# Performance work log

Hardware: AMD Instinct MI355X
Metric: run time of the kernel (lower is better)

## Reference

```python
import jax, jax.numpy as jnp
import numpy as np

IT = 3  # BP iterations
ROWS, N = 144, 576  # H dims: wman_N0576_R34 -> 144 checks, 576 vars
ROW_DEG = 6  # check-node degree


def _make_H():
    rng = np.random.default_rng(0)
    H = np.zeros((ROWS, N), np.float32)
    for i in range(ROWS):
        cols = rng.choice(N, size=ROW_DEG, replace=False)
        H[i, cols] = 1.0
    return jnp.asarray(H)


def _quantize(x, eta, qk):
    # 4-level soft quantization: softmax over -(x-qk)^2/(2 eta^2)
    logits = -(x[..., None] - qk) ** 2 / (2.0 * eta ** 2 + 1e-12)
    w = jax.nn.softmax(logits, axis=-1)
    return jnp.sum(w * qk, axis=-1)


def setup_inputs() -> dict:
    key = jax.random.key(0)
    k1, = jax.random.split(key, 1)
    batch = 512
    r = jax.random.normal(k1, (batch, N), dtype=jnp.float32)
    H = _make_H()
    alpha = jnp.ones((IT,), jnp.float32) * 0.7
    beta = jnp.ones((IT,), jnp.float32) * 0.05
    eta = jnp.ones((IT,), jnp.float32) * 0.7
    qk = jnp.linspace(-4.0, 4.0, 4).astype(jnp.float32)
    return {"r": r, "H": H, "alpha": alpha, "beta": beta, "eta": eta, "qk": qk}


def reference(r, H, alpha, beta, eta, qk):
    B, n = r.shape
    Hmask = H == 1
    node_idx = jnp.arange(n)[None, None, :]
    M = H[None] * r[:, None, :]          # (B, ROWS, N)
    E = jnp.zeros_like(M)
    for t in range(IT):
        # --- check-to-variable (min-sum with masked top-2) ---
        masked_abs = jnp.where(Hmask, jnp.abs(M), jnp.inf)
        neg_top, idx = jax.lax.top_k(-masked_abs, 2)  # two smallest
        min1 = -neg_top[..., 0:1]
        min2 = -neg_top[..., 1:2]
        idx1 = idx[..., 0:1]
        E_abs = jnp.where(node_idx == idx1, min2, min1)
        signs = jnp.sign(M)
        valid_signs = jnp.where(Hmask, signs, 1.0)
        row_sign_prod = jnp.prod(valid_signs, axis=2, keepdims=True)
        E_sign = row_sign_prod * valid_signs
        E = alpha[t] * E_sign * jnp.maximum(0.0, E_abs - beta[t])
        E = E * H
        E = _quantize(E, eta[t], qk)
        # --- variable-to-check update ---
        sum_E = jnp.sum(E, axis=1, keepdims=True)
        M = (r[:, None, :] + sum_E - E) * H[None]
        M = _quantize(M, eta[t], qk)
    return r + jnp.sum(E, axis=1)
```

## Files before the change

kernel.cpp:

```cpp
#include <hip/hip_runtime.h>
#include <math.h>

#define IT 3
#define ROWS 144
#define NCOLS 576
#define ROW_DEG 6

__device__ __forceinline__ float quantize1(float x, float S,
                                           float K0, float K1, float K2, float K3,
                                           float KQ0, float KQ1, float KQ2, float KQ3) {
    float s = fminf(fmaxf(x * S, -30.0f), 30.0f);
    float B = __expf(s);
    float den = ((K3 * B + K2) * B + K1) * B + K0;
    float num = ((KQ3 * B + KQ2) * B + KQ1) * B + KQ0;
    return num * __builtin_amdgcn_rcpf(den);
}

__device__ __forceinline__ float signf(float x) {
    return (x > 0.0f) ? 1.0f : ((x < 0.0f) ? -1.0f : 0.0f);
}

__global__ __launch_bounds__(64) void extract_cols_kernel(
    const float* __restrict__ H, int* __restrict__ cols)
{
    const int row  = blockIdx.x;
    const int lane = threadIdx.x;
    float hv[9];
    #pragma unroll
    for (int i = 0; i < 9; ++i) hv[i] = H[row * NCOLS + i * 64 + lane];
    int base = 0;
    #pragma unroll
    for (int i = 0; i < 9; ++i) {
        bool nz = hv[i] != 0.0f;
        unsigned long long mask = __ballot(nz);
        if (nz) {
            int rank = base + __popcll(mask & ((1ull << lane) - 1ull));
            if (rank < ROW_DEG) cols[row * ROW_DEG + rank] = i * 64 + lane;
        }
        base += __popcll(mask);
    }
}

__global__ __launch_bounds__(64) void decode_kernel(
    const float* __restrict__ r, const int* __restrict__ cols,
    const float* __restrict__ alpha, const float* __restrict__ beta,
    const float* __restrict__ eta, const float* __restrict__ qk,
    float* __restrict__ out)
{
    __shared__ __align__(16) float s_r[NCOLS];
    __shared__ __align__(16) float s_sumE[NCOLS];

    const int b    = blockIdx.x;
    const int lane = threadIdx.x;

    const float q0 = qk[0], q1 = qk[1], q2 = qk[2], q3 = qk[3];

    const float4* rb4 = reinterpret_cast<const float4*>(r + (size_t)b * NCOLS);
    float4* s_r4 = reinterpret_cast<float4*>(s_r);
    #pragma unroll
    for (int p = 0; p < 3; ++p) {
        int j = lane + 64 * p;
        if (j < NCOLS / 4) s_r4[j] = rb4[j];
    }

    const float dq = (q3 - q0) * (1.0f / 3.0f);
    float al[IT], be[IT], sc[IT];
    float k0[IT], k1[IT], k2[IT], k3[IT];
    #pragma unroll
    for (int t = 0; t < IT; ++t) {
        al[t] = alpha[t];
        be[t] = beta[t];
        float inv2e = 1.0f / (2.0f * eta[t] * eta[t] + 1e-12f);
        sc[t] = 2.0f * dq * inv2e;
        k0[t] = __expf(-q0 * q0 * inv2e);
        k1[t] = __expf(-q1 * q1 * inv2e);
        k2[t] = __expf(-q2 * q2 * inv2e);
        k3[t] = __expf(-q3 * q3 * inv2e);
    }

    const bool act2 = lane < (ROWS - 128);

    int   c[3][ROW_DEG];
    float m[3][ROW_DEG];
    float E[3][ROW_DEG];

    __syncthreads();

    #pragma unroll
    for (int p = 0; p < 3; ++p) {
        if (p == 2 && !act2) continue;
        const int row = lane + 64 * p;
        #pragma unroll
        for (int e = 0; e < ROW_DEG; ++e) {
            c[p][e] = cols[row * ROW_DEG + e];
            m[p][e] = s_r[c[p][e]];
        }
    }

    #pragma unroll
    for (int t = 0; t < IT; ++t) {
        __syncthreads();
        #pragma unroll
        for (int p = 0; p < 9; ++p) s_sumE[lane + 64 * p] = 0.0f;
        __syncthreads();

        const float A = al[t], Bt = be[t], S = sc[t];
        const float K0 = k0[t], K1 = k1[t], K2 = k2[t], K3 = k3[t];
        const float KQ0 = K0 * q0, KQ1 = K1 * q1, KQ2 = K2 * q2, KQ3 = K3 * q3;

        #pragma unroll
        for (int p = 0; p < 3; ++p) {
            if (p == 2 && !act2) continue;
            float min1 = INFINITY, min2 = INFINITY;
            int idx = -1;
            float sp = 1.0f;
            #pragma unroll
            for (int e = 0; e < ROW_DEG; ++e) {
                float a = fabsf(m[p][e]);
                sp *= signf(m[p][e]);
                if (a < min1) { min2 = min1; min1 = a; idx = e; }
                else if (a < min2) { min2 = a; }
            }
            #pragma unroll
            for (int e = 0; e < ROW_DEG; ++e) {
                float eabs = (e == idx) ? min2 : min1;
                float v = A * sp * signf(m[p][e]) * fmaxf(0.0f, eabs - Bt);
                v = quantize1(v, S, K0, K1, K2, K3, KQ0, KQ1, KQ2, KQ3);
                E[p][e] = v;
                atomicAdd(&s_sumE[c[p][e]], v);
            }
        }
        __syncthreads();

        if (t < IT - 1) {
            #pragma unroll
            for (int p = 0; p < 3; ++p) {
                if (p == 2 && !act2) continue;
                #pragma unroll
                for (int e = 0; e < ROW_DEG; ++e) {
                    float v = s_r[c[p][e]] + s_sumE[c[p][e]] - E[p][e];
                    m[p][e] = quantize1(v, S, K0, K1, K2, K3, KQ0, KQ1, KQ2, KQ3);
                }
            }
        }
    }

    float4* ob4 = reinterpret_cast<float4*>(out + (size_t)b * NCOLS);
    float4* s_s4 = reinterpret_cast<float4*>(s_sumE);
    #pragma unroll
    for (int p = 0; p < 3; ++p) {
        int j = lane + 64 * p;
        if (j < NCOLS / 4) {
            float4 rv = s_r4[j], sv = s_s4[j];
            float4 o;
            o.x = rv.x + sv.x; o.y = rv.y + sv.y;
            o.z = rv.z + sv.z; o.w = rv.w + sv.w;
            ob4[j] = o;
        }
    }
}

extern "C" void kernel_launch(void* const* d_in, const int* in_sizes, int n_in,
                              void* d_out, int out_size, void* d_ws, size_t ws_size,
                              hipStream_t stream) {
    const float* r     = (const float*)d_in[0];
    const float* H     = (const float*)d_in[1];
    const float* alpha = (const float*)d_in[2];
    const float* beta  = (const float*)d_in[3];
    const float* eta   = (const float*)d_in[4];
    const float* qk    = (const float*)d_in[5];
    float* out = (float*)d_out;

    int* cols = (int*)d_ws;
    const int batch = in_sizes[0] / NCOLS;

    hipLaunchKernelGGL(extract_cols_kernel, dim3(ROWS), dim3(64), 0, stream,
                       H, cols);
    hipLaunchKernelGGL(decode_kernel, dim3(batch), dim3(64), 0, stream,
                       r, cols, alpha, beta, eta, qk, out);
}
```

Baseline: 77.87 us.

## Double-buffer sum array, pad dummy rows, and cache gathered r values

Replaces the single shared sum buffer with two ping-pong buffers so that clearing the next buffer overlaps the variable update, which drops one barrier per iteration. Pads the shared arrays so the 48 inactive lanes in the third row group work on dummy columns instead of branching. Keeps the gathered r values in registers and precomputes the two magnitude factors per row. The cost is more shared memory, register pressure, and extra atomics from the dummy lanes.

```diff
diff --git a/kernel.cpp b/kernel.cpp
--- a/kernel.cpp
+++ b/kernel.cpp
@@ -5,6 +5,7 @@
 #define ROWS 144
 #define NCOLS 576
 #define ROW_DEG 6
+#define PADN 896
 
 __device__ __forceinline__ float quantize1(float x, float S,
                                            float K0, float K1, float K2, float K3,
@@ -47,13 +48,11 @@
     const float* __restrict__ eta, const float* __restrict__ qk,
     float* __restrict__ out)
 {
-    __shared__ __align__(16) float s_r[NCOLS];
-    __shared__ __align__(16) float s_sumE[NCOLS];
+    __shared__ __align__(16) float s_r[PADN];
+    __shared__ __align__(16) float s_sum[2][PADN];
 
     const int b    = blockIdx.x;
     const int lane = threadIdx.x;
-
-    const float q0 = qk[0], q1 = qk[1], q2 = qk[2], q3 = qk[3];
 
     const float4* rb4 = reinterpret_cast<const float4*>(r + (size_t)b * NCOLS);
     float4* s_r4 = reinterpret_cast<float4*>(s_r);
@@ -62,7 +61,12 @@
         int j = lane + 64 * p;
         if (j < NCOLS / 4) s_r4[j] = rb4[j];
     }
+    #pragma unroll
+    for (int p = 0; p < (PADN - NCOLS) / 64; ++p) s_r[NCOLS + lane + 64 * p] = 0.0f;
+    #pragma unroll
+    for (int p = 0; p < PADN / 64; ++p) s_sum[0][lane + 64 * p] = 0.0f;
 
+    const float q0 = qk[0], q1 = qk[1], q2 = qk[2], q3 = qk[3];
     const float dq = (q3 - q0) * (1.0f / 3.0f);
     float al[IT], be[IT], sc[IT];
     float k0[IT], k1[IT], k2[IT], k3[IT];
@@ -78,39 +82,39 @@
         k3[t] = __expf(-q3 * q3 * inv2e);
     }
 
-    const bool act2 = lane < (ROWS - 128);
-
-    int   c[3][ROW_DEG];
-    float m[3][ROW_DEG];
-    float E[3][ROW_DEG];
+    int c[3][ROW_DEG];
+    #pragma unroll
+    for (int p = 0; p < 3; ++p) {
+        const int row  = lane + 64 * p;
+        const bool real = row < ROWS;
+        const int lrow = real ? row : 0;
+        #pragma unroll
+        for (int e = 0; e < ROW_DEG; ++e) {
+            int cr = cols[lrow * ROW_DEG + e];
+            c[p][e] = real ? cr : (NCOLS + (lane - 16) * ROW_DEG + e);
+        }
+    }
 
     __syncthreads();
 
+    float rc[3][ROW_DEG], m[3][ROW_DEG], E[3][ROW_DEG];
     #pragma unroll
-    for (int p = 0; p < 3; ++p) {
-        if (p == 2 && !act2) continue;
-        const int row = lane + 64 * p;
+    for (int p = 0; p < 3; ++p)
         #pragma unroll
         for (int e = 0; e < ROW_DEG; ++e) {
-            c[p][e] = cols[row * ROW_DEG + e];
-            m[p][e] = s_r[c[p][e]];
+            rc[p][e] = s_r[c[p][e]];
+            m[p][e]  = rc[p][e];
         }
-    }
 
     #pragma unroll
     for (int t = 0; t < IT; ++t) {
-        __syncthreads();
-        #pragma unroll
-        for (int p = 0; p < 9; ++p) s_sumE[lane + 64 * p] = 0.0f;
-        __syncthreads();
-
+        const int cur = t & 1, nxt = cur ^ 1;
         const float A = al[t], Bt = be[t], S = sc[t];
         const float K0 = k0[t], K1 = k1[t], K2 = k2[t], K3 = k3[t];
         const float KQ0 = K0 * q0, KQ1 = K1 * q1, KQ2 = K2 * q2, KQ3 = K3 * q3;
 
         #pragma unroll
         for (int p = 0; p < 3; ++p) {
-            if (p == 2 && !act2) continue;
             float min1 = INFINITY, min2 = INFINITY;
             int idx = -1;
             float sp = 1.0f;
@@ -121,32 +125,35 @@
                 if (a < min1) { min2 = min1; min1 = a; idx = e; }
                 else if (a < min2) { min2 = a; }
             }
+            const float f1 = A * sp * fmaxf(0.0f, min1 - Bt);
+            const float f2 = A * sp * fmaxf(0.0f, min2 - Bt);
             #pragma unroll
             for (int e = 0; e < ROW_DEG; ++e) {
-                float eabs = (e == idx) ? min2 : min1;
-                float v = A * sp * signf(m[p][e]) * fmaxf(0.0f, eabs - Bt);
+                float v = signf(m[p][e]) * ((e == idx) ? f2 : f1);
                 v = quantize1(v, S, K0, K1, K2, K3, KQ0, KQ1, KQ2, KQ3);
                 E[p][e] = v;
-                atomicAdd(&s_sumE[c[p][e]], v);
+                atomicAdd(&s_sum[cur][c[p][e]], v);
             }
         }
         __syncthreads();
 
         if (t < IT - 1) {
             #pragma unroll
-            for (int p = 0; p < 3; ++p) {
-                if (p == 2 && !act2) continue;
+            for (int p = 0; p < PADN / 64; ++p) s_sum[nxt][lane + 64 * p] = 0.0f;
+            #pragma unroll
+            for (int p = 0; p < 3; ++p)
                 #pragma unroll
                 for (int e = 0; e < ROW_DEG; ++e) {
-                    float v = s_r[c[p][e]] + s_sumE[c[p][e]] - E[p][e];
+                    float v = rc[p][e] + s_sum[cur][c[p][e]] - E[p][e];
                     m[p][e] = quantize1(v, S, K0, K1, K2, K3, KQ0, KQ1, KQ2, KQ3);
                 }
-            }
+            __syncthreads();
         }
     }
 
     float4* ob4 = reinterpret_cast<float4*>(out + (size_t)b * NCOLS);
-    float4* s_s4 = reinterpret_cast<float4*>(s_sumE);
+    const float4* s_s4 = reinterpret_cast<const float4*>(s_sum[0]);
+    __syncthreads();
     #pragma unroll
     for (int p = 0; p < 3; ++p) {
         int j = lane + 64 * p;
```

Measured after the change: 80.24 us. +3.0%, slower.
